# Optimization experiments

Measured on AMD Instinct MI355X. Metric: run time of the kernel, lower is better.

Reference implementation:

```python
import jax, jax.numpy as jnp
import numpy as np

B, N, QD = 2, 4096, 512
HEADS, DIM_HEAD = 8, 64
INNER = HEADS * DIM_HEAD  # 512
SCALE = DIM_HEAD ** -0.5


def setup_inputs() -> dict:
    key = jax.random.key(0)
    ks = jax.random.split(key, 6)
    s = 0.02
    return {
        "x": jax.random.normal(ks[0], (B, N, QD), dtype=jnp.float32),
        "Wq": jax.random.normal(ks[1], (QD, INNER), dtype=jnp.float32) * s,
        "Wk": jax.random.normal(ks[2], (QD, INNER), dtype=jnp.float32) * s,
        "Wv": jax.random.normal(ks[3], (QD, INNER), dtype=jnp.float32) * s,
        "Wo": jax.random.normal(ks[4], (INNER, QD), dtype=jnp.float32) * s,
        "bo": jnp.zeros((QD,), dtype=jnp.float32),
    }


def reference(x, Wq, Wk, Wv, Wo, bo):
    # self-attention: context = x; mask = None; attention_sf = False
    q = x @ Wq  # [B, N, INNER]
    k = x @ Wk
    v = x @ Wv
    # split heads: [B, H, N, D]
    def split(t):
        return t.reshape(B, N, HEADS, DIM_HEAD).transpose(0, 2, 1, 3)
    q, k, v = split(q), split(k), split(v)
    # fp32 QK^T (ATTN_PRECISION='fp32' path)
    sim = jnp.einsum('bhid,bhjd->bhij', q.astype(jnp.float32), k.astype(jnp.float32)) * SCALE
    attn = jax.nn.softmax(sim, axis=-1)
    out = jnp.einsum('bhij,bhjd->bhid', attn, v)  # [B, H, N, D]
    out = out.transpose(0, 2, 1, 3).reshape(B, N, INNER)
    return out @ Wo + bo  # Dropout(p=0) is identity
```

## Files before the change

kernel.cpp:

```cpp
#include <hip/hip_runtime.h>
#include <hip/hip_bf16.h>


typedef __attribute__((ext_vector_type(8))) short short8;
typedef __attribute__((ext_vector_type(4))) float floatx4;

#define MFMA16(a, b, c) __builtin_amdgcn_mfma_f32_16x16x32_bf16((a), (b), (c), 0, 0, 0)

#if __has_builtin(__builtin_amdgcn_exp2f)
#define EXP2(x) __builtin_amdgcn_exp2f(x)
#else
#define EXP2(x) exp2f(x)
#endif

#define QSCALE 0.18033688011112042f

static __device__ __forceinline__ unsigned short f2b(float f) {
  unsigned int u = __float_as_uint(f);
  u += 0x7FFFu + ((u >> 16) & 1u);
  return (unsigned short)(u >> 16);
}

static __device__ __forceinline__ unsigned int pkb(float a, float b) {
  float2 t{a, b};
  __hip_bfloat162 h = __float22bfloat162_rn(t);
  union { __hip_bfloat162 h2; unsigned int u; } cv;
  cv.h2 = h;
  return cv.u;
}

static __device__ __forceinline__ void dma16(const unsigned short* g,
                                             unsigned short* l) {
  __builtin_amdgcn_global_load_lds(
      (const __attribute__((address_space(1))) unsigned int*)g,
      (__attribute__((address_space(3))) unsigned int*)l, 16, 0, 0);
}

__global__ __launch_bounds__(256) void wt_cvt_kernel(
    const float* __restrict__ Wq, const float* __restrict__ Wk,
    const float* __restrict__ Wv, const float* __restrict__ Wo,
    unsigned short* __restrict__ wtq, unsigned short* __restrict__ wtk,
    unsigned short* __restrict__ wtv, unsigned short* __restrict__ wto) {
  const int z = blockIdx.z;
  const float* __restrict__ W = (z == 0) ? Wq : (z == 1) ? Wk : (z == 2) ? Wv : Wo;
  unsigned short* __restrict__ T = (z == 0) ? wtq : (z == 1) ? wtk : (z == 2) ? wtv : wto;
  const int k0 = blockIdx.x * 32, c0 = blockIdx.y * 32;
  __shared__ float Ts[32][33];
  const int tid = threadIdx.x;
  const int r = tid >> 3, cc = (tid & 7) * 4;
  const float4 v = *(const float4*)(W + (k0 + r) * 512 + c0 + cc);
  Ts[r][cc] = v.x; Ts[r][cc + 1] = v.y; Ts[r][cc + 2] = v.z; Ts[r][cc + 3] = v.w;
  __syncthreads();
  const unsigned long long uu =
      (unsigned long long)pkb(Ts[cc][r], Ts[cc + 1][r]) |
      ((unsigned long long)pkb(Ts[cc + 2][r], Ts[cc + 3][r]) << 32);
  *(unsigned long long*)(T + (c0 + r) * 512 + k0 + cc) = uu;
}

__global__ __launch_bounds__(256) void x_cvt_kernel(
    const float* __restrict__ x, unsigned short* __restrict__ xb) {
  const int idx = (blockIdx.x * 256 + threadIdx.x) * 8;
  const float4 a = *(const float4*)(x + idx);
  const float4 b = *(const float4*)(x + idx + 4);
  unsigned int u[4] = {pkb(a.x, a.y), pkb(a.z, a.w), pkb(b.x, b.y),
                       pkb(b.z, b.w)};
  *(short8*)(xb + idx) = *(short8*)u;
}

__global__ __launch_bounds__(256) void qkv_proj_kernel(
    const unsigned short* __restrict__ xb, const unsigned short* __restrict__ wtq,
    const unsigned short* __restrict__ wtk,
    const unsigned short* __restrict__ wtv, unsigned short* __restrict__ qo,
    unsigned short* __restrict__ ko, unsigned short* __restrict__ vo) {
  const int z = blockIdx.z;
  const unsigned short* __restrict__ wt = (z == 0) ? wtq : (z == 1) ? wtk : wtv;
  const int m0 = blockIdx.x * 128;
  const int c0 = blockIdx.y * 128;
  __shared__ __align__(16) unsigned short As[128 * 32];
  __shared__ __align__(16) unsigned short Bs[128 * 32];
  const int tid = threadIdx.x;
  const int lane = tid & 63, w = tid >> 6;
  const int i = lane & 15, q = lane >> 4;
  const int wy = w >> 1, wx = w & 1;
  const int sr = lane >> 2, sc8 = (lane & 3) * 8;
  const unsigned short* ag = xb + (m0 + w * 32 + sr) * 512 + sc8;
  const unsigned short* bg = wt + (c0 + w * 32 + sr) * 512 + sc8;
  unsigned short* adst0 = &As[(w * 32) * 32];
  unsigned short* adst1 = &As[(w * 32 + 16) * 32];
  unsigned short* bdst0 = &Bs[(w * 32) * 32];
  unsigned short* bdst1 = &Bs[(w * 32 + 16) * 32];
  floatx4 acc[4][4] = {};
  for (int k0 = 0; k0 < 512; k0 += 32) {
    dma16(ag + k0, adst0);
    dma16(ag + 16 * 512 + k0, adst1);
    dma16(bg + k0, bdst0);
    dma16(bg + 16 * 512 + k0, bdst1);
    __syncthreads();
    short8 af[4], bfr[4];
#pragma unroll
    for (int t = 0; t < 4; ++t)
      af[t] = *(const short8*)&As[(wy * 64 + t * 16 + i) * 32 + q * 8];
#pragma unroll
    for (int g = 0; g < 4; ++g)
      bfr[g] = *(const short8*)&Bs[(wx * 64 + g * 16 + i) * 32 + q * 8];
#pragma unroll
    for (int t = 0; t < 4; ++t)
#pragma unroll
      for (int g = 0; g < 4; ++g) acc[t][g] = MFMA16(af[t], bfr[g], acc[t][g]);
    __syncthreads();
  }
#pragma unroll
  for (int t = 0; t < 4; ++t)
#pragma unroll
    for (int g = 0; g < 4; ++g) {
      const int col = c0 + wx * 64 + g * 16 + i;
      const int h = col >> 6, d = col & 63;
      const int row0 = m0 + wy * 64 + t * 16 + q * 4;
      const int b = row0 >> 12;
      const int n0 = row0 & 4095;
      if (z == 2) {
        unsigned int* dst =
            (unsigned int*)&vo[(((b * 8 + h) * 64 + d) << 12) + n0];
        dst[0] = pkb(acc[t][g][0], acc[t][g][1]);
        dst[1] = pkb(acc[t][g][2], acc[t][g][3]);
      } else {
        unsigned short* dst = (z == 0) ? qo : ko;
        const float sc = (z == 0) ? QSCALE : 1.0f;
#pragma unroll
        for (int r = 0; r < 4; ++r)
          dst[(((b * 8 + h) << 12) + (n0 + r)) * 64 + d] =
              f2b(acc[t][g][r] * sc);
      }
    }
}

__global__ __launch_bounds__(512, 4) void flash_kernel(
    const unsigned short* __restrict__ Q, const unsigned short* __restrict__ K,
    const unsigned short* __restrict__ Vt, unsigned short* __restrict__ O) {
  const int bh = blockIdx.x;
  const int m0 = blockIdx.y * 128;
  const int tid = threadIdx.x;
  const int lane = tid & 63, w = tid >> 6;
  const int i = lane & 15, q = lane >> 4;
  const int rt = w & 3;
  const int kg = w >> 2;
  const unsigned short* qp = Q + bh * (4096 * 64);
  const unsigned short* kp = K + bh * (4096 * 64);
  const unsigned short* vp = Vt + bh * (64 * 4096);

  __shared__ __align__(16) unsigned short SM[32768];
  unsigned short* Ks = SM + kg * 4096;
  unsigned short* Vs = SM + 8192 + kg * 4096;
  unsigned short* pw = SM + 16384 + w * 2048;

  const int srow = (tid & 255) >> 3;
  const int c0s = tid & 7;
  const int sw8 = (c0s ^ (srow & 7)) * 8;
  const unsigned short* kgp = kp + (kg * 2048 + srow) * 64 + c0s * 8;
  const unsigned short* vgp = vp + srow * 4096 + kg * 2048 + c0s * 8;

  short8 qf[2][2];
#pragma unroll
  for (int t = 0; t < 2; ++t)
#pragma unroll
    for (int kc = 0; kc < 2; ++kc)
      qf[t][kc] = *(const short8*)(qp + (m0 + rt * 32 + t * 16 + i) * 64 +
                                   kc * 32 + q * 8);

  floatx4 accO[2][4] = {};
  floatx4 accL[2] = {};
  short8 ones;
  {
    const short ov = (i == 0) ? (short)0x3F80 : (short)0;
#pragma unroll
    for (int j = 0; j < 8; ++j) ones[j] = ov;
  }
  const floatx4 zf = {0.f, 0.f, 0.f, 0.f};
  const int sl = i & 7;

  *(short8*)&Ks[srow * 64 + sw8] = *(const short8*)(kgp);
  *(short8*)&Ks[(srow + 32) * 64 + sw8] = *(const short8*)(kgp + 32 * 64);
  *(short8*)&Vs[srow * 64 + sw8] = *(const short8*)(vgp);
  *(short8*)&Vs[(srow + 32) * 64 + sw8] = *(const short8*)(vgp + 32 * 4096);
  __syncthreads();

  for (int jt = 0; jt < 32; ++jt) {
    short8 kn0, kn1, vn0, vn1;
    if (jt < 31) {
      kn0 = *(const short8*)(kgp + (jt + 1) * 4096);
      kn1 = *(const short8*)(kgp + (jt + 1) * 4096 + 32 * 64);
      vn0 = *(const short8*)(vgp + (jt + 1) * 64);
      vn1 = *(const short8*)(vgp + (jt + 1) * 64 + 32 * 4096);
    }
#pragma unroll
    for (int g = 0; g < 4; ++g) {
      const short8 kf0 = *(const short8*)(&Ks[(g * 16 + i) * 64 + (q ^ sl) * 8]);
      const short8 kf1 =
          *(const short8*)(&Ks[(g * 16 + i) * 64 + ((4 + q) ^ sl) * 8]);
#pragma unroll
      for (int t = 0; t < 2; ++t) {
        floatx4 s = MFMA16(kf0, qf[t][0], zf);
        s = MFMA16(kf1, qf[t][1], s);
        const float e0 = EXP2(s[0]), e1 = EXP2(s[1]);
        const float e2 = EXP2(s[2]), e3 = EXP2(s[3]);
        *(unsigned long long*)&pw[(t * 16 + i) * 64 +
                                  (((2 * g + (q >> 1)) ^ sl) * 8) +
                                  (q & 1) * 4] =
            (unsigned long long)pkb(e0, e1) |
            ((unsigned long long)pkb(e2, e3) << 32);
      }
    }
    short8 pf[2][2];
#pragma unroll
    for (int t = 0; t < 2; ++t) {
      pf[t][0] = *(const short8*)(pw + (t * 16 + i) * 64 + (q ^ sl) * 8);
      pf[t][1] = *(const short8*)(pw + (t * 16 + i) * 64 + ((4 + q) ^ sl) * 8);
      accL[t] = MFMA16(pf[t][0], ones, accL[t]);
      accL[t] = MFMA16(pf[t][1], ones, accL[t]);
    }
#pragma unroll
    for (int dg = 0; dg < 4; ++dg) {
      const short8 vf0 =
          *(const short8*)(&Vs[(dg * 16 + i) * 64 + (q ^ sl) * 8]);
      const short8 vf1 =
          *(const short8*)(&Vs[(dg * 16 + i) * 64 + ((4 + q) ^ sl) * 8]);
#pragma unroll
      for (int t = 0; t < 2; ++t) {
        accO[t][dg] = MFMA16(pf[t][0], vf0, accO[t][dg]);
        accO[t][dg] = MFMA16(pf[t][1], vf1, accO[t][dg]);
      }
    }
    __syncthreads();
    if (jt < 31) {
      *(short8*)&Ks[srow * 64 + sw8] = kn0;
      *(short8*)&Ks[(srow + 32) * 64 + sw8] = kn1;
      *(short8*)&Vs[srow * 64 + sw8] = vn0;
      *(short8*)&Vs[(srow + 32) * 64 + sw8] = vn1;
    }
    __syncthreads();
  }

  float* MB = (float*)SM;
  if (kg == 1) {
    float* dst = MB + (rt * 64 + lane) * 40;
#pragma unroll
    for (int t = 0; t < 2; ++t) {
#pragma unroll
      for (int dg = 0; dg < 4; ++dg)
#pragma unroll
        for (int r = 0; r < 4; ++r) dst[t * 16 + dg * 4 + r] = accO[t][dg][r];
#pragma unroll
      for (int r = 0; r < 4; ++r) dst[32 + t * 4 + r] = accL[t][r];
    }
  }
  __syncthreads();
  if (kg == 1) return;
  {
    const float* src = MB + (rt * 64 + lane) * 40;
#pragma unroll
    for (int t = 0; t < 2; ++t) {
#pragma unroll
      for (int dg = 0; dg < 4; ++dg)
#pragma unroll
        for (int r = 0; r < 4; ++r) accO[t][dg][r] += src[t * 16 + dg * 4 + r];
#pragma unroll
      for (int r = 0; r < 4; ++r) accL[t][r] += src[32 + t * 4 + r];
    }
  }

  const int b = bh >> 3, h = bh & 7;
#pragma unroll
  for (int t = 0; t < 2; ++t) {
    float inv[4];
#pragma unroll
    for (int r = 0; r < 4; ++r) {
      const float l = __shfl(accL[t][r], lane & 48, 64);
      inv[r] = 1.0f / l;
    }
#pragma unroll
    for (int dg = 0; dg < 4; ++dg)
#pragma unroll
      for (int r = 0; r < 4; ++r) {
        const int n = m0 + rt * 32 + t * 16 + q * 4 + r;
        const int col = h * 64 + dg * 16 + i;
        O[((b << 12) + n) * 512 + col] = f2b(accO[t][dg][r] * inv[r]);
      }
  }
}

__global__ __launch_bounds__(256) void out_proj_kernel(
    const unsigned short* __restrict__ A, const unsigned short* __restrict__ wto,
    const float* __restrict__ bo, float* __restrict__ out) {
  const int m0 = blockIdx.x * 64, c0 = blockIdx.y * 64;
  __shared__ __align__(16) unsigned short As[64 * 32];
  __shared__ __align__(16) unsigned short Bs[64 * 32];
  const int tid = threadIdx.x;
  const int lane = tid & 63, w = tid >> 6;
  const int i = lane & 15, q = lane >> 4;
  const int wy = w >> 1, wx = w & 1;
  const int sr = lane >> 2, sc8 = (lane & 3) * 8;
  const unsigned short* ag = A + (m0 + w * 16 + sr) * 512 + sc8;
  const unsigned short* bg = wto + (c0 + w * 16 + sr) * 512 + sc8;
  unsigned short* adst = &As[(w * 16) * 32];
  unsigned short* bdst = &Bs[(w * 16) * 32];
  floatx4 acc[2][2] = {};
  for (int k0 = 0; k0 < 512; k0 += 32) {
    dma16(ag + k0, adst);
    dma16(bg + k0, bdst);
    __syncthreads();
    short8 af[2], bfr[2];
#pragma unroll
    for (int t = 0; t < 2; ++t)
      af[t] = *(const short8*)&As[(wy * 32 + t * 16 + i) * 32 + q * 8];
#pragma unroll
    for (int g = 0; g < 2; ++g)
      bfr[g] = *(const short8*)&Bs[(wx * 32 + g * 16 + i) * 32 + q * 8];
#pragma unroll
    for (int t = 0; t < 2; ++t)
#pragma unroll
      for (int g = 0; g < 2; ++g) acc[t][g] = MFMA16(af[t], bfr[g], acc[t][g]);
    __syncthreads();
  }
#pragma unroll
  for (int t = 0; t < 2; ++t)
#pragma unroll
    for (int g = 0; g < 2; ++g) {
      const int col = c0 + wx * 32 + g * 16 + i;
      const float bias = bo[col];
#pragma unroll
      for (int r = 0; r < 4; ++r) {
        const int row = m0 + wy * 32 + t * 16 + q * 4 + r;
        out[row * 512 + col] = acc[t][g][r] + bias;
      }
    }
}

extern "C" void kernel_launch(void* const* d_in, const int* in_sizes, int n_in,
                              void* d_out, int out_size, void* d_ws,
                              size_t ws_size, hipStream_t stream) {
  const float* x = (const float*)d_in[0];
  const float* Wq = (const float*)d_in[1];
  const float* Wk = (const float*)d_in[2];
  const float* Wv = (const float*)d_in[3];
  const float* Wo = (const float*)d_in[4];
  const float* bo = (const float*)d_in[5];
  float* out = (float*)d_out;

  const size_t tsz = (size_t)16 * 4096 * 64;
  unsigned short* qws = (unsigned short*)d_ws;
  unsigned short* kws = qws + tsz;
  unsigned short* vws = kws + tsz;
  unsigned short* ows = vws + tsz;
  unsigned short* wtq = ows + tsz;
  unsigned short* wtk = wtq + 512 * 512;
  unsigned short* wtv = wtk + 512 * 512;
  unsigned short* wto = wtv + 512 * 512;
  unsigned short* xb = wto + 512 * 512;

  wt_cvt_kernel<<<dim3(16, 16, 4), 256, 0, stream>>>(Wq, Wk, Wv, Wo, wtq, wtk,
                                                     wtv, wto);
  x_cvt_kernel<<<2048, 256, 0, stream>>>(x, xb);
  qkv_proj_kernel<<<dim3(64, 4, 3), 256, 0, stream>>>(xb, wtq, wtk, wtv, qws,
                                                      kws, vws);
  flash_kernel<<<dim3(16, 32), 512, 0, stream>>>(qws, kws, vws, ows);
  out_proj_kernel<<<dim3(128, 8), 256, 0, stream>>>(ows, wto, bo, out);
}
```

Before: 198.0 us.

## Merge prep kernels and fuse x conversion into a joint QKV projection

The weight-transpose and x-to-bf16 conversions now run in one launch, and the three separate Q/K/V projection grids become one kernel. Each block loads one fp32 x tile, converts it to bf16 in registers, stores it into padded shared memory, and multiplies it against all three weight tiles. This drops a launch and reads each x tile once per column block instead of once per projection. In exchange, x is read as fp32 with scalar loads instead of async DMA, and the prep kernel still writes xb even though the fused kernel no longer reads it.

Result: no change. 194.3 us (-1.9%).

```diff
diff --git a/kernel.cpp b/kernel.cpp
--- a/kernel.cpp
+++ b/kernel.cpp
@@ -36,17 +36,28 @@
       (__attribute__((address_space(3))) unsigned int*)l, 16, 0, 0);
 }
 
-__global__ __launch_bounds__(256) void wt_cvt_kernel(
+__global__ __launch_bounds__(256) void prep_kernel(
     const float* __restrict__ Wq, const float* __restrict__ Wk,
     const float* __restrict__ Wv, const float* __restrict__ Wo,
-    unsigned short* __restrict__ wtq, unsigned short* __restrict__ wtk,
-    unsigned short* __restrict__ wtv, unsigned short* __restrict__ wto) {
+    const float* __restrict__ x, unsigned short* __restrict__ wtq,
+    unsigned short* __restrict__ wtk, unsigned short* __restrict__ wtv,
+    unsigned short* __restrict__ wto, unsigned short* __restrict__ xb) {
   const int z = blockIdx.z;
+  const int tid = threadIdx.x;
+  if (z >= 4) {
+    const int bid = (z - 4) * 256 + blockIdx.y * 16 + blockIdx.x;
+    const int idx = (bid * 256 + tid) * 8;
+    const float4 a = *(const float4*)(x + idx);
+    const float4 b = *(const float4*)(x + idx + 4);
+    unsigned int u[4] = {pkb(a.x, a.y), pkb(a.z, a.w), pkb(b.x, b.y),
+                         pkb(b.z, b.w)};
+    *(short8*)(xb + idx) = *(short8*)u;
+    return;
+  }
   const float* __restrict__ W = (z == 0) ? Wq : (z == 1) ? Wk : (z == 2) ? Wv : Wo;
   unsigned short* __restrict__ T = (z == 0) ? wtq : (z == 1) ? wtk : (z == 2) ? wtv : wto;
   const int k0 = blockIdx.x * 32, c0 = blockIdx.y * 32;
   __shared__ float Ts[32][33];
-  const int tid = threadIdx.x;
   const int r = tid >> 3, cc = (tid & 7) * 4;
   const float4 v = *(const float4*)(W + (k0 + r) * 512 + c0 + cc);
   Ts[r][cc] = v.x; Ts[r][cc + 1] = v.y; Ts[r][cc + 2] = v.z; Ts[r][cc + 3] = v.w;
@@ -57,81 +68,82 @@
   *(unsigned long long*)(T + (c0 + r) * 512 + k0 + cc) = uu;
 }
 
-__global__ __launch_bounds__(256) void x_cvt_kernel(
-    const float* __restrict__ x, unsigned short* __restrict__ xb) {
-  const int idx = (blockIdx.x * 256 + threadIdx.x) * 8;
-  const float4 a = *(const float4*)(x + idx);
-  const float4 b = *(const float4*)(x + idx + 4);
-  unsigned int u[4] = {pkb(a.x, a.y), pkb(a.z, a.w), pkb(b.x, b.y),
-                       pkb(b.z, b.w)};
-  *(short8*)(xb + idx) = *(short8*)u;
-}
-
-__global__ __launch_bounds__(256) void qkv_proj_kernel(
-    const unsigned short* __restrict__ xb, const unsigned short* __restrict__ wtq,
+__global__ __launch_bounds__(256) void qkv_fused_kernel(
+    const float* __restrict__ x, const unsigned short* __restrict__ wtq,
     const unsigned short* __restrict__ wtk,
     const unsigned short* __restrict__ wtv, unsigned short* __restrict__ qo,
     unsigned short* __restrict__ ko, unsigned short* __restrict__ vo) {
-  const int z = blockIdx.z;
-  const unsigned short* __restrict__ wt = (z == 0) ? wtq : (z == 1) ? wtk : wtv;
   const int m0 = blockIdx.x * 128;
-  const int c0 = blockIdx.y * 128;
-  __shared__ __align__(16) unsigned short As[128 * 32];
-  __shared__ __align__(16) unsigned short Bs[128 * 32];
+  const int c0 = blockIdx.y * 64;
+  __shared__ __align__(16) unsigned short As[128 * 40];
+  __shared__ __align__(16) unsigned short Bs[3][64 * 32];
   const int tid = threadIdx.x;
   const int lane = tid & 63, w = tid >> 6;
   const int i = lane & 15, q = lane >> 4;
   const int wy = w >> 1, wx = w & 1;
-  const int sr = lane >> 2, sc8 = (lane & 3) * 8;
-  const unsigned short* ag = xb + (m0 + w * 32 + sr) * 512 + sc8;
-  const unsigned short* bg = wt + (c0 + w * 32 + sr) * 512 + sc8;
-  unsigned short* adst0 = &As[(w * 32) * 32];
-  unsigned short* adst1 = &As[(w * 32 + 16) * 32];
-  unsigned short* bdst0 = &Bs[(w * 32) * 32];
-  unsigned short* bdst1 = &Bs[(w * 32 + 16) * 32];
-  floatx4 acc[4][4] = {};
+  const int arow = tid >> 1, ch = (tid & 1) * 16;
+  const int br = w * 16 + (lane >> 2), bc8 = (lane & 3) * 8;
+  const unsigned short* bg0 = wtq + (c0 + br) * 512 + bc8;
+  const unsigned short* bg1 = wtk + (c0 + br) * 512 + bc8;
+  const unsigned short* bg2 = wtv + (c0 + br) * 512 + bc8;
+  unsigned short* bd0 = &Bs[0][(w * 16) * 32];
+  unsigned short* bd1 = &Bs[1][(w * 16) * 32];
+  unsigned short* bd2 = &Bs[2][(w * 16) * 32];
+  floatx4 acc[3][4][2] = {};
   for (int k0 = 0; k0 < 512; k0 += 32) {
-    dma16(ag + k0, adst0);
-    dma16(ag + 16 * 512 + k0, adst1);
-    dma16(bg + k0, bdst0);
-    dma16(bg + 16 * 512 + k0, bdst1);
-    __syncthreads();
-    short8 af[4], bfr[4];
+    dma16(bg0 + k0, bd0);
+    dma16(bg1 + k0, bd1);
+    dma16(bg2 + k0, bd2);
+    {
+      const float* src = x + (m0 + arow) * 512 + k0 + ch;
+      unsigned int av[8];
+#pragma unroll
+      for (int j = 0; j < 8; ++j) av[j] = pkb(src[2 * j], src[2 * j + 1]);
+      *(short8*)&As[arow * 40 + ch] = *(short8*)&av[0];
+      *(short8*)&As[arow * 40 + ch + 8] = *(short8*)&av[4];
+    }
+    __syncthreads();
+    short8 af[4];
 #pragma unroll
     for (int t = 0; t < 4; ++t)
-      af[t] = *(const short8*)&As[(wy * 64 + t * 16 + i) * 32 + q * 8];
-#pragma unroll
-    for (int g = 0; g < 4; ++g)
-      bfr[g] = *(const short8*)&Bs[(wx * 64 + g * 16 + i) * 32 + q * 8];
+      af[t] = *(const short8*)&As[(wy * 64 + t * 16 + i) * 40 + q * 8];
+#pragma unroll
+    for (int z = 0; z < 3; ++z)
+#pragma unroll
+      for (int g = 0; g < 2; ++g) {
+        const short8 bf =
+            *(const short8*)&Bs[z][(wx * 32 + g * 16 + i) * 32 + q * 8];
+#pragma unroll
+        for (int t = 0; t < 4; ++t)
+          acc[z][t][g] = MFMA16(af[t], bf, acc[z][t][g]);
+      }
+    __syncthreads();
+  }
+#pragma unroll
+  for (int z = 0; z < 3; ++z)
 #pragma unroll
     for (int t = 0; t < 4; ++t)
 #pragma unroll
-      for (int g = 0; g < 4; ++g) acc[t][g] = MFMA16(af[t], bfr[g], acc[t][g]);
-    __syncthreads();
-  }
-#pragma unroll
-  for (int t = 0; t < 4; ++t)
-#pragma unroll
-    for (int g = 0; g < 4; ++g) {
-      const int col = c0 + wx * 64 + g * 16 + i;
-      const int h = col >> 6, d = col & 63;
-      const int row0 = m0 + wy * 64 + t * 16 + q * 4;
-      const int b = row0 >> 12;
-      const int n0 = row0 & 4095;
-      if (z == 2) {
-        unsigned int* dst =
-            (unsigned int*)&vo[(((b * 8 + h) * 64 + d) << 12) + n0];
-        dst[0] = pkb(acc[t][g][0], acc[t][g][1]);
-        dst[1] = pkb(acc[t][g][2], acc[t][g][3]);
-      } else {
-        unsigned short* dst = (z == 0) ? qo : ko;
-        const float sc = (z == 0) ? QSCALE : 1.0f;
-#pragma unroll
-        for (int r = 0; r < 4; ++r)
-          dst[(((b * 8 + h) << 12) + (n0 + r)) * 64 + d] =
-              f2b(acc[t][g][r] * sc);
-      }
-    }
+      for (int g = 0; g < 2; ++g) {
+        const int col = c0 + wx * 32 + g * 16 + i;
+        const int h = col >> 6, d = col & 63;
+        const int row0 = m0 + wy * 64 + t * 16 + q * 4;
+        const int b = row0 >> 12;
+        const int n0 = row0 & 4095;
+        if (z == 2) {
+          unsigned int* dst =
+              (unsigned int*)&vo[(((b * 8 + h) * 64 + d) << 12) + n0];
+          dst[0] = pkb(acc[z][t][g][0], acc[z][t][g][1]);
+          dst[1] = pkb(acc[z][t][g][2], acc[z][t][g][3]);
+        } else {
+          unsigned short* dst = (z == 0) ? qo : ko;
+          const float sc = (z == 0) ? QSCALE : 1.0f;
+#pragma unroll
+          for (int r = 0; r < 4; ++r)
+            dst[(((b * 8 + h) << 12) + (n0 + r)) * 64 + d] =
+                f2b(acc[z][t][g][r] * sc);
+        }
+      }
 }
 
 __global__ __launch_bounds__(512, 4) void flash_kernel(
@@ -357,11 +369,10 @@
   unsigned short* wto = wtv + 512 * 512;
   unsigned short* xb = wto + 512 * 512;
 
-  wt_cvt_kernel<<<dim3(16, 16, 4), 256, 0, stream>>>(Wq, Wk, Wv, Wo, wtq, wtk,
-                                                     wtv, wto);
-  x_cvt_kernel<<<2048, 256, 0, stream>>>(x, xb);
-  qkv_proj_kernel<<<dim3(64, 4, 3), 256, 0, stream>>>(xb, wtq, wtk, wtv, qws,
-                                                      kws, vws);
+  prep_kernel<<<dim3(16, 16, 12), 256, 0, stream>>>(Wq, Wk, Wv, Wo, x, wtq,
+                                                    wtk, wtv, wto, xb);
+  qkv_fused_kernel<<<dim3(64, 8), 256, 0, stream>>>(x, wtq, wtk, wtv, qws, kws,
+                                                    vws);
   flash_kernel<<<dim3(16, 32), 512, 0, stream>>>(qws, kws, vws, ows);
   out_proj_kernel<<<dim3(128, 8), 256, 0, stream>>>(ows, wto, bo, out);
 }
```
